# Kernel tuning notes

Hardware: AMD Instinct MI355X
Metric: run time of the kernel (lower is better)

## Reference

```python
import jax, jax.numpy as jnp
import numpy as np

N_NODES = 100000
N_EDGES = 1600000
NODES_PER_GRAPH = 100  # equal-sized graphs -> batch = arange // 100
POOL_K = 30


def setup_inputs() -> dict:
    key = jax.random.key(0)
    ks = jax.random.split(key, 8)
    F_IN, H1, H2, OUT = 128, 128, 128, 64
    x = jax.random.normal(ks[0], (N_NODES, F_IN), dtype=jnp.float32)
    edge_index = jax.random.randint(ks[1], (2, N_EDGES), 0, N_NODES, dtype=jnp.int64)
    batch = (jnp.arange(N_NODES, dtype=jnp.int64) // NODES_PER_GRAPH)
    # Glorot-ish init for weights, zero bias (as PyG GCNConv defaults)
    W1 = jax.random.normal(ks[2], (F_IN, H1), dtype=jnp.float32) / np.sqrt(F_IN)
    b1 = jnp.zeros((H1,), dtype=jnp.float32)
    W2 = jax.random.normal(ks[3], (H1, H2), dtype=jnp.float32) / np.sqrt(H1)
    b2 = jnp.zeros((H2,), dtype=jnp.float32)
    W3 = jax.random.normal(ks[4], (H2, OUT), dtype=jnp.float32) / np.sqrt(H2)
    b3 = jnp.zeros((OUT,), dtype=jnp.float32)
    return {"x": x, "edge_index": edge_index, "batch": batch,
            "W1": W1, "b1": b1, "W2": W2, "b2": b2, "W3": W3, "b3": b3}


def _gcn_conv(x, src, dst, W, b):
    """PyG GCNConv: xW, add self-loops, symmetric D^-1/2 A D^-1/2 scatter-add, +bias."""
    n = x.shape[0]
    loops = jnp.arange(n, dtype=src.dtype)
    row = jnp.concatenate([src, loops])  # message source
    col = jnp.concatenate([dst, loops])  # aggregation target
    xw = x @ W
    deg = jax.ops.segment_sum(jnp.ones(col.shape[0], x.dtype), col, num_segments=n)
    dinv = jnp.where(deg > 0, jax.lax.rsqrt(deg), 0.0)
    norm = dinv[row] * dinv[col]  # [E+N]
    out = jax.ops.segment_sum(xw[row] * norm[:, None], col, num_segments=n)
    return out + b


def _sort_pool(x, k):
    """global_sort_pool: per-graph descending sort by last channel, take top-k, flatten.
    Graphs are equal-sized and contiguous, so reshape to [B, P, C]."""
    n, c = x.shape
    xb = x.reshape(n // NODES_PER_GRAPH, NODES_PER_GRAPH, c)  # [B, P, C]
    order = jnp.argsort(-xb[..., -1], axis=1)[:, :k]          # [B, k]
    topk = jnp.take_along_axis(xb, order[..., None], axis=1)  # [B, k, C]
    return topk.reshape(topk.shape[0], k * c)


def reference(x, edge_index, batch, W1, b1, W2, b2, W3, b3):
    src, dst = edge_index[0], edge_index[1]
    h = jax.nn.relu(_gcn_conv(x, src, dst, W1, b1))
    h = jax.nn.relu(_gcn_conv(h, src, dst, W2, b2))
    h = _gcn_conv(h, src, dst, W3, b3)
    return _sort_pool(h, POOL_K)
```

## Files before the change

### kernel.cpp

```cpp
#include <hip/hip_runtime.h>
#include <math.h>

static inline size_t ws_align(size_t x) { return (x + 255) & ~(size_t)255; }

__global__ void count_kernel(const int* __restrict__ dst, int* __restrict__ counts, int E) {
  int e = blockIdx.x * 256 + threadIdx.x;
  if (e < E) atomicAdd(&counts[dst[e]], 1);
}

__global__ __launch_bounds__(1024) void scan_kernel(const int* __restrict__ counts,
    int* __restrict__ offsets, int* __restrict__ cursor, double* __restrict__ dinv, int n) {
  __shared__ int warpsums[16];
  __shared__ int s_carry;
  int tid = threadIdx.x;
  int lane = tid & 63, wid = tid >> 6;
  if (tid == 0) s_carry = 0;
  __syncthreads();
  for (int base = 0; base < n; base += 1024) {
    int i = base + tid;
    int v = (i < n) ? counts[i] : 0;
    int x = v;
    #pragma unroll
    for (int d = 1; d < 64; d <<= 1) {
      int y = __shfl_up(x, d, 64);
      if (lane >= d) x += y;
    }
    if (lane == 63) warpsums[wid] = x;
    __syncthreads();
    if (wid == 0) {
      int w = (lane < 16) ? warpsums[lane] : 0;
      #pragma unroll
      for (int d = 1; d < 16; d <<= 1) {
        int y = __shfl_up(w, d, 64);
        if (lane >= d) w += y;
      }
      if (lane < 16) warpsums[lane] = w;
    }
    __syncthreads();
    int excl = s_carry + x - v + (wid > 0 ? warpsums[wid - 1] : 0);
    if (i < n) {
      offsets[i] = excl;
      cursor[i] = excl;
      dinv[i] = 1.0 / sqrt((double)(v + 1));
    }
    __syncthreads();
    if (tid == 0) s_carry += warpsums[15];
    __syncthreads();
  }
  if (tid == 0) offsets[n] = s_carry;
}

__global__ void scatter_kernel(const int* __restrict__ src, const int* __restrict__ dst,
    int* __restrict__ cursor, int* __restrict__ srcs, int E) {
  int e = blockIdx.x * 256 + threadIdx.x;
  if (e < E) {
    int p = atomicAdd(&cursor[dst[e]], 1);
    srcs[p] = src[e];
  }
}

template<int H>
__global__ __launch_bounds__(256) void gemm_kernel(const float* __restrict__ X,
    const float* __restrict__ W, float* __restrict__ out, int N) {
  __shared__ float xs[128][68];
  const int tid  = threadIdx.x;
  const int row0 = blockIdx.x * 64;
  #pragma unroll
  for (int p = 0; p < 8; ++p) {
    int idx = p * 256 + tid;
    int r = idx >> 5;
    int c4 = idx & 31;
    int grow = row0 + r;
    float4 v = make_float4(0.f, 0.f, 0.f, 0.f);
    if (grow < N) v = *(const float4*)(X + (size_t)grow * 128 + c4 * 4);
    xs[c4 * 4 + 0][r] = v.x;
    xs[c4 * 4 + 1][r] = v.y;
    xs[c4 * 4 + 2][r] = v.z;
    xs[c4 * 4 + 3][r] = v.w;
  }
  __syncthreads();
  constexpr int CPT = H / 16;
  const int rowg = tid & 15;
  const int colg = tid >> 4;
  double acc[4][CPT];
  #pragma unroll
  for (int j = 0; j < 4; ++j)
    #pragma unroll
    for (int h = 0; h < CPT; ++h) acc[j][h] = 0.0;

  #pragma unroll 4
  for (int k = 0; k < 128; k += 2) {
    float4 av0 = *(const float4*)(&xs[k][rowg * 4]);
    float4 av1 = *(const float4*)(&xs[k + 1][rowg * 4]);
    double a0[4], a1[4];
    a0[0] = (double)av0.x; a0[1] = (double)av0.y; a0[2] = (double)av0.z; a0[3] = (double)av0.w;
    a1[0] = (double)av1.x; a1[1] = (double)av1.y; a1[2] = (double)av1.z; a1[3] = (double)av1.w;
    double b0[CPT], b1[CPT];
    const float* w0 = W + (size_t)k * H + colg * CPT;
    const float* w1 = w0 + H;
    #pragma unroll
    for (int q = 0; q < CPT / 4; ++q) {
      float4 v0 = *(const float4*)(w0 + q * 4);
      float4 v1 = *(const float4*)(w1 + q * 4);
      b0[q*4+0] = (double)v0.x; b0[q*4+1] = (double)v0.y;
      b0[q*4+2] = (double)v0.z; b0[q*4+3] = (double)v0.w;
      b1[q*4+0] = (double)v1.x; b1[q*4+1] = (double)v1.y;
      b1[q*4+2] = (double)v1.z; b1[q*4+3] = (double)v1.w;
    }
    #pragma unroll
    for (int j = 0; j < 4; ++j)
      #pragma unroll
      for (int h = 0; h < CPT; ++h) {
        acc[j][h] = fma(a0[j], b0[h], acc[j][h]);
        acc[j][h] = fma(a1[j], b1[h], acc[j][h]);
      }
  }
  #pragma unroll
  for (int j = 0; j < 4; ++j) {
    int grow = row0 + rowg * 4 + j;
    if (grow < N) {
      float* o = out + (size_t)grow * H + colg * CPT;
      #pragma unroll
      for (int q = 0; q < CPT / 4; ++q) {
        float4 v = make_float4((float)acc[j][q*4+0], (float)acc[j][q*4+1],
                               (float)acc[j][q*4+2], (float)acc[j][q*4+3]);
        *(float4*)(o + q * 4) = v;
      }
    }
  }
}

template<int C, bool RELU>
__global__ __launch_bounds__(256) void gather_kernel(const float* __restrict__ xw,
    const double* __restrict__ dinv, const int* __restrict__ offs,
    const int* __restrict__ srcs, const float* __restrict__ bias,
    float* __restrict__ out, int N) {
  constexpr int LPR = C / 4;
  constexpr int EPI = 64 / LPR;
  const int node = blockIdx.x * 4 + (threadIdx.x >> 6);
  if (node >= N) return;
  const int lane = threadIdx.x & 63;
  const int grp  = lane / LPR;
  const int l    = lane % LPR;
  const int c0   = l * 4;
  const int e0 = offs[node], e1 = offs[node + 1];
  const double di = dinv[node];
  double a0 = 0.0, a1 = 0.0, a2 = 0.0, a3 = 0.0;

  for (int base = e0; base < e1; base += 4 * EPI) {
    int ss[4];
    #pragma unroll
    for (int u = 0; u < 4; ++u) {
      int ee = base + u * EPI + grp;
      ss[u] = srcs[ee < e1 ? ee : e1 - 1];
    }
    float4 vv[4];
    double ww[4];
    #pragma unroll
    for (int u = 0; u < 4; ++u) {
      vv[u] = *(const float4*)(xw + (size_t)ss[u] * C + c0);
      ww[u] = dinv[ss[u]];
    }
    #pragma unroll
    for (int u = 0; u < 4; ++u) {
      int ee = base + u * EPI + grp;
      double w = (ee < e1) ? ww[u] : 0.0;
      a0 = fma(w, (double)vv[u].x, a0);
      a1 = fma(w, (double)vv[u].y, a1);
      a2 = fma(w, (double)vv[u].z, a2);
      a3 = fma(w, (double)vv[u].w, a3);
    }
  }
  #pragma unroll
  for (int m = LPR; m < 64; m <<= 1) {
    a0 += __shfl_xor(a0, m, 64);
    a1 += __shfl_xor(a1, m, 64);
    a2 += __shfl_xor(a2, m, 64);
    a3 += __shfl_xor(a3, m, 64);
  }
  if (grp == 0) {
    const double d2 = di * di;
    float4 sv = *(const float4*)(xw + (size_t)node * C + c0);
    float4 bv = *(const float4*)(bias + c0);
    double o0 = fma(di, a0, fma(d2, (double)sv.x, (double)bv.x));
    double o1 = fma(di, a1, fma(d2, (double)sv.y, (double)bv.y));
    double o2 = fma(di, a2, fma(d2, (double)sv.z, (double)bv.z));
    double o3 = fma(di, a3, fma(d2, (double)sv.w, (double)bv.w));
    if (RELU) {
      o0 = o0 > 0.0 ? o0 : 0.0; o1 = o1 > 0.0 ? o1 : 0.0;
      o2 = o2 > 0.0 ? o2 : 0.0; o3 = o3 > 0.0 ? o3 : 0.0;
    }
    *(float4*)(out + (size_t)node * C + c0) =
        make_float4((float)o0, (float)o1, (float)o2, (float)o3);
  }
}

__global__ __launch_bounds__(128) void sortpool_kernel(const float* __restrict__ h,
    float* __restrict__ out) {
  __shared__ float sv[128];
  __shared__ int si[128];
  int g = blockIdx.x;
  int tid = threadIdx.x;
  const float* hg = h + (size_t)g * 100 * 64;
  if (tid < 100) {
    sv[tid] = hg[tid * 64 + 63];
    si[tid] = tid;
  } else {
    sv[tid] = -3.0e38f;
    si[tid] = 1 << 30;
  }
  __syncthreads();
  for (int k = 2; k <= 128; k <<= 1) {
    for (int j = k >> 1; j > 0; j >>= 1) {
      int i = tid;
      int l = i ^ j;
      if (l > i) {
        float va = sv[i], vb = sv[l];
        int ia = si[i], ib = si[l];
        bool a_before_b = (va > vb) || (va == vb && ia < ib);
        bool up = ((i & k) == 0);
        bool sw = up ? !a_before_b : a_before_b;
        if (sw) { sv[i] = vb; sv[l] = va; si[i] = ib; si[l] = ia; }
      }
      __syncthreads();
    }
  }
  for (int t = tid; t < 30 * 64; t += 128) {
    int kk = t >> 6;
    int c = t & 63;
    out[(size_t)g * (30 * 64) + t] = hg[si[kk] * 64 + c];
  }
}

extern "C" void kernel_launch(void* const* d_in, const int* in_sizes, int n_in,
                              void* d_out, int out_size, void* d_ws, size_t ws_size,
                              hipStream_t stream) {
  const float* x  = (const float*)d_in[0];
  const int*   ei = (const int*)d_in[1];
  const float* W1 = (const float*)d_in[3];
  const float* b1 = (const float*)d_in[4];
  const float* W2 = (const float*)d_in[5];
  const float* b2 = (const float*)d_in[6];
  const float* W3 = (const float*)d_in[7];
  const float* b3 = (const float*)d_in[8];

  const int N = in_sizes[0] / 128;
  const int E = in_sizes[1] / 2;
  const int* src = ei;
  const int* dst = ei + E;
  (void)n_in; (void)out_size; (void)ws_size;

  char* ws = (char*)d_ws;
  size_t off = 0;
  auto alloc = [&](size_t bytes) { char* p = ws + off; off = ws_align(off + bytes); return p; };
  float*  xw      = (float*) alloc((size_t)N * 128 * 4);
  float*  h       = (float*) alloc((size_t)N * 128 * 4);
  double* dinv    = (double*)alloc((size_t)N * 8);
  int*    offsets = (int*)   alloc(((size_t)N + 1) * 4);
  int*    cursor  = (int*)   alloc((size_t)N * 4);
  int*    counts  = (int*)   alloc((size_t)N * 4);
  int*    srcs    = (int*)   alloc((size_t)E * 4);

  hipMemsetAsync(counts, 0, (size_t)N * 4, stream);
  count_kernel<<<(E + 255) / 256, 256, 0, stream>>>(dst, counts, E);
  scan_kernel<<<1, 1024, 0, stream>>>(counts, offsets, cursor, dinv, N);
  scatter_kernel<<<(E + 255) / 256, 256, 0, stream>>>(src, dst, cursor, srcs, E);

  const int gblocks  = (N + 63) / 64;
  const int nblocks4 = (N + 3) / 4;

  gemm_kernel<128><<<gblocks, 256, 0, stream>>>(x, W1, xw, N);
  gather_kernel<128, true ><<<nblocks4, 256, 0, stream>>>(xw, dinv, offsets, srcs, b1, h, N);
  gemm_kernel<128><<<gblocks, 256, 0, stream>>>(h, W2, xw, N);
  gather_kernel<128, true ><<<nblocks4, 256, 0, stream>>>(xw, dinv, offsets, srcs, b2, h, N);
  gemm_kernel<64 ><<<gblocks, 256, 0, stream>>>(h, W3, xw, N);
  gather_kernel<64,  false><<<nblocks4, 256, 0, stream>>>(xw, dinv, offsets, srcs, b3, h, N);
  sortpool_kernel<<<N / 100, 128, 0, stream>>>(h, (float*)d_out);
}
```

Measured before the change: 995.0 us.

## Parallelize CSR scan, precompute edge weights, pre-convert weights to double, unroll gather

```diff
diff --git a/kernel.cpp b/kernel.cpp
--- a/kernel.cpp
+++ b/kernel.cpp
@@ -8,60 +8,95 @@
   if (e < E) atomicAdd(&counts[dst[e]], 1);
 }
 
-__global__ __launch_bounds__(1024) void scan_kernel(const int* __restrict__ counts,
-    int* __restrict__ offsets, int* __restrict__ cursor, double* __restrict__ dinv, int n) {
+__global__ __launch_bounds__(256) void scanA_kernel(const int* __restrict__ counts,
+    int* __restrict__ bsums, int n) {
+  __shared__ int red[4];
+  const int base = blockIdx.x * 1024;
+  const int tid = threadIdx.x;
+  int s = 0;
+  #pragma unroll
+  for (int u = 0; u < 4; ++u) {
+    int i = base + u * 256 + tid;
+    s += (i < n) ? counts[i] : 0;
+  }
+  #pragma unroll
+  for (int m = 1; m < 64; m <<= 1) s += __shfl_xor(s, m, 64);
+  if ((tid & 63) == 0) red[tid >> 6] = s;
+  __syncthreads();
+  if (tid == 0) bsums[blockIdx.x] = red[0] + red[1] + red[2] + red[3];
+}
+
+__global__ __launch_bounds__(128) void scanB_kernel(int* __restrict__ bsums, int nb) {
+  __shared__ int tmp[129];
+  int tid = threadIdx.x;
+  tmp[tid] = (tid < nb) ? bsums[tid] : 0;
+  __syncthreads();
+  if (tid == 0) {
+    int run = 0;
+    for (int i = 0; i < nb; ++i) { int v = tmp[i]; tmp[i] = run; run += v; }
+  }
+  __syncthreads();
+  if (tid < nb) bsums[tid] = tmp[tid];
+}
+
+__global__ __launch_bounds__(1024) void scanC_kernel(const int* __restrict__ counts,
+    const int* __restrict__ bsums, int* __restrict__ offsets, int* __restrict__ cursor,
+    double* __restrict__ dinv, int n) {
   __shared__ int warpsums[16];
-  __shared__ int s_carry;
-  int tid = threadIdx.x;
-  int lane = tid & 63, wid = tid >> 6;
-  if (tid == 0) s_carry = 0;
-  __syncthreads();
-  for (int base = 0; base < n; base += 1024) {
-    int i = base + tid;
-    int v = (i < n) ? counts[i] : 0;
-    int x = v;
-    #pragma unroll
-    for (int d = 1; d < 64; d <<= 1) {
-      int y = __shfl_up(x, d, 64);
-      if (lane >= d) x += y;
-    }
-    if (lane == 63) warpsums[wid] = x;
-    __syncthreads();
-    if (wid == 0) {
-      int w = (lane < 16) ? warpsums[lane] : 0;
-      #pragma unroll
-      for (int d = 1; d < 16; d <<= 1) {
-        int y = __shfl_up(w, d, 64);
-        if (lane >= d) w += y;
-      }
-      if (lane < 16) warpsums[lane] = w;
-    }
-    __syncthreads();
-    int excl = s_carry + x - v + (wid > 0 ? warpsums[wid - 1] : 0);
-    if (i < n) {
-      offsets[i] = excl;
-      cursor[i] = excl;
-      dinv[i] = 1.0 / sqrt((double)(v + 1));
-    }
-    __syncthreads();
-    if (tid == 0) s_carry += warpsums[15];
-    __syncthreads();
-  }
-  if (tid == 0) offsets[n] = s_carry;
+  const int tid = threadIdx.x;
+  const int lane = tid & 63, wid = tid >> 6;
+  const int i = blockIdx.x * 1024 + tid;
+  int v = (i < n) ? counts[i] : 0;
+  int x = v;
+  #pragma unroll
+  for (int d = 1; d < 64; d <<= 1) {
+    int y = __shfl_up(x, d, 64);
+    if (lane >= d) x += y;
+  }
+  if (lane == 63) warpsums[wid] = x;
+  __syncthreads();
+  if (wid == 0) {
+    int w = (lane < 16) ? warpsums[lane] : 0;
+    #pragma unroll
+    for (int d = 1; d < 16; d <<= 1) {
+      int y = __shfl_up(w, d, 64);
+      if (lane >= d) w += y;
+    }
+    if (lane < 16) warpsums[lane] = w;
+  }
+  __syncthreads();
+  int excl = bsums[blockIdx.x] + x - v + (wid > 0 ? warpsums[wid - 1] : 0);
+  if (i < n) {
+    offsets[i] = excl;
+    cursor[i] = excl;
+    dinv[i] = 1.0 / sqrt((double)(v + 1));
+    if (i == n - 1) offsets[n] = excl + v;
+  }
 }
 
 __global__ void scatter_kernel(const int* __restrict__ src, const int* __restrict__ dst,
-    int* __restrict__ cursor, int* __restrict__ srcs, int E) {
+    int* __restrict__ cursor, int* __restrict__ srcs, double* __restrict__ ew,
+    const double* __restrict__ dinv, int E, int use_ew) {
   int e = blockIdx.x * 256 + threadIdx.x;
   if (e < E) {
-    int p = atomicAdd(&cursor[dst[e]], 1);
-    srcs[p] = src[e];
-  }
+    int s = src[e], d = dst[e];
+    int p = atomicAdd(&cursor[d], 1);
+    srcs[p] = s;
+    if (use_ew) ew[p] = dinv[s] * dinv[d];
+  }
+}
+
+__global__ void cvtW_kernel(const float* __restrict__ W1, const float* __restrict__ W2,
+    const float* __restrict__ W3, double* __restrict__ W1d, double* __restrict__ W2d,
+    double* __restrict__ W3d) {
+  int i = blockIdx.x * 256 + threadIdx.x;
+  if (i < 16384) { W1d[i] = (double)W1[i]; W2d[i] = (double)W2[i]; }
+  if (i < 8192)  { W3d[i] = (double)W3[i]; }
 }
 
 template<int H>
 __global__ __launch_bounds__(256) void gemm_kernel(const float* __restrict__ X,
-    const float* __restrict__ W, float* __restrict__ out, int N) {
+    const double* __restrict__ Wd, float* __restrict__ out, int N) {
   __shared__ float xs[128][68];
   const int tid  = threadIdx.x;
   const int row0 = blockIdx.x * 64;
@@ -88,7 +123,7 @@
     #pragma unroll
     for (int h = 0; h < CPT; ++h) acc[j][h] = 0.0;
 
-  #pragma unroll 4
+  #pragma unroll 2
   for (int k = 0; k < 128; k += 2) {
     float4 av0 = *(const float4*)(&xs[k][rowg * 4]);
     float4 av1 = *(const float4*)(&xs[k + 1][rowg * 4]);
@@ -96,16 +131,14 @@
     a0[0] = (double)av0.x; a0[1] = (double)av0.y; a0[2] = (double)av0.z; a0[3] = (double)av0.w;
     a1[0] = (double)av1.x; a1[1] = (double)av1.y; a1[2] = (double)av1.z; a1[3] = (double)av1.w;
     double b0[CPT], b1[CPT];
-    const float* w0 = W + (size_t)k * H + colg * CPT;
-    const float* w1 = w0 + H;
-    #pragma unroll
-    for (int q = 0; q < CPT / 4; ++q) {
-      float4 v0 = *(const float4*)(w0 + q * 4);
-      float4 v1 = *(const float4*)(w1 + q * 4);
-      b0[q*4+0] = (double)v0.x; b0[q*4+1] = (double)v0.y;
-      b0[q*4+2] = (double)v0.z; b0[q*4+3] = (double)v0.w;
-      b1[q*4+0] = (double)v1.x; b1[q*4+1] = (double)v1.y;
-      b1[q*4+2] = (double)v1.z; b1[q*4+3] = (double)v1.w;
+    const double* w0 = Wd + (size_t)k * H + colg * CPT;
+    const double* w1 = w0 + H;
+    #pragma unroll
+    for (int q = 0; q < CPT / 2; ++q) {
+      double2 v0 = *(const double2*)(w0 + q * 2);
+      double2 v1 = *(const double2*)(w1 + q * 2);
+      b0[q*2+0] = v0.x; b0[q*2+1] = v0.y;
+      b1[q*2+0] = v1.x; b1[q*2+1] = v1.y;
     }
     #pragma unroll
     for (int j = 0; j < 4; ++j)
@@ -130,39 +163,41 @@
   }
 }
 
-template<int C, bool RELU>
+template<int C, bool RELU, bool USE_EW>
 __global__ __launch_bounds__(256) void gather_kernel(const float* __restrict__ xw,
     const double* __restrict__ dinv, const int* __restrict__ offs,
-    const int* __restrict__ srcs, const float* __restrict__ bias,
-    float* __restrict__ out, int N) {
+    const int* __restrict__ srcs, const double* __restrict__ ew,
+    const float* __restrict__ bias, float* __restrict__ out, int N) {
   constexpr int LPR = C / 4;
   constexpr int EPI = 64 / LPR;
+  constexpr int U = 8;
   const int node = blockIdx.x * 4 + (threadIdx.x >> 6);
   if (node >= N) return;
   const int lane = threadIdx.x & 63;
   const int grp  = lane / LPR;
-  const int l    = lane % LPR;
-  const int c0   = l * 4;
+  const int c0   = (lane % LPR) * 4;
   const int e0 = offs[node], e1 = offs[node + 1];
   const double di = dinv[node];
   double a0 = 0.0, a1 = 0.0, a2 = 0.0, a3 = 0.0;
 
-  for (int base = e0; base < e1; base += 4 * EPI) {
-    int ss[4];
-    #pragma unroll
-    for (int u = 0; u < 4; ++u) {
+  for (int base = e0; base < e1; base += U * EPI) {
+    int ss[U];
+    double ww[U];
+    float4 vv[U];
+    #pragma unroll
+    for (int u = 0; u < U; ++u) {
       int ee = base + u * EPI + grp;
-      ss[u] = srcs[ee < e1 ? ee : e1 - 1];
-    }
-    float4 vv[4];
-    double ww[4];
-    #pragma unroll
-    for (int u = 0; u < 4; ++u) {
+      int cl = ee < e1 ? ee : e1 - 1;
+      ss[u] = srcs[cl];
+      if (USE_EW) ww[u] = ew[cl];
+    }
+    #pragma unroll
+    for (int u = 0; u < U; ++u) {
       vv[u] = *(const float4*)(xw + (size_t)ss[u] * C + c0);
-      ww[u] = dinv[ss[u]];
-    }
-    #pragma unroll
-    for (int u = 0; u < 4; ++u) {
+      if (!USE_EW) ww[u] = dinv[ss[u]];
+    }
+    #pragma unroll
+    for (int u = 0; u < U; ++u) {
       int ee = base + u * EPI + grp;
       double w = (ee < e1) ? ww[u] : 0.0;
       a0 = fma(w, (double)vv[u].x, a0);
@@ -182,10 +217,18 @@
     const double d2 = di * di;
     float4 sv = *(const float4*)(xw + (size_t)node * C + c0);
     float4 bv = *(const float4*)(bias + c0);
-    double o0 = fma(di, a0, fma(d2, (double)sv.x, (double)bv.x));
-    double o1 = fma(di, a1, fma(d2, (double)sv.y, (double)bv.y));
-    double o2 = fma(di, a2, fma(d2, (double)sv.z, (double)bv.z));
-    double o3 = fma(di, a3, fma(d2, (double)sv.w, (double)bv.w));
+    double o0, o1, o2, o3;
+    if (USE_EW) {
+      o0 = a0 + fma(d2, (double)sv.x, (double)bv.x);
+      o1 = a1 + fma(d2, (double)sv.y, (double)bv.y);
+      o2 = a2 + fma(d2, (double)sv.z, (double)bv.z);
+      o3 = a3 + fma(d2, (double)sv.w, (double)bv.w);
+    } else {
+      o0 = fma(di, a0, fma(d2, (double)sv.x, (double)bv.x));
+      o1 = fma(di, a1, fma(d2, (double)sv.y, (double)bv.y));
+      o2 = fma(di, a2, fma(d2, (double)sv.z, (double)bv.z));
+      o3 = fma(di, a3, fma(d2, (double)sv.w, (double)bv.w));
+    }
     if (RELU) {
       o0 = o0 > 0.0 ? o0 : 0.0; o1 = o1 > 0.0 ? o1 : 0.0;
       o2 = o2 > 0.0 ? o2 : 0.0; o3 = o3 > 0.0 ? o3 : 0.0;
@@ -248,7 +291,9 @@
   const int E = in_sizes[1] / 2;
   const int* src = ei;
   const int* dst = ei + E;
-  (void)n_in; (void)out_size; (void)ws_size;
+  (void)n_in; (void)out_size;
+
+  const int nb = (N + 1023) / 1024;
 
   char* ws = (char*)d_ws;
   size_t off = 0;
@@ -260,20 +305,37 @@
   int*    cursor  = (int*)   alloc((size_t)N * 4);
   int*    counts  = (int*)   alloc((size_t)N * 4);
   int*    srcs    = (int*)   alloc((size_t)E * 4);
+  double* W1d     = (double*)alloc(16384 * 8);
+  double* W2d     = (double*)alloc(16384 * 8);
+  double* W3d     = (double*)alloc(8192 * 8);
+  int*    bsums   = (int*)   alloc((size_t)(nb + 1) * 4);
+  double* ew      = (double*)alloc((size_t)E * 8);
+  const bool use_ew = (off <= ws_size);
 
   hipMemsetAsync(counts, 0, (size_t)N * 4, stream);
   count_kernel<<<(E + 255) / 256, 256, 0, stream>>>(dst, counts, E);
-  scan_kernel<<<1, 1024, 0, stream>>>(counts, offsets, cursor, dinv, N);
-  scatter_kernel<<<(E + 255) / 256, 256, 0, stream>>>(src, dst, cursor, srcs, E);
+  scanA_kernel<<<nb, 256, 0, stream>>>(counts, bsums, N);
+  scanB_kernel<<<1, 128, 0, stream>>>(bsums, nb);
+  scanC_kernel<<<nb, 1024, 0, stream>>>(counts, bsums, offsets, cursor, dinv, N);
+  scatter_kernel<<<(E + 255) / 256, 256, 0, stream>>>(src, dst, cursor, srcs, ew, dinv, E, use_ew ? 1 : 0);
+  cvtW_kernel<<<64, 256, 0, stream>>>(W1, W2, W3, W1d, W2d, W3d);
 
   const int gblocks  = (N + 63) / 64;
   const int nblocks4 = (N + 3) / 4;
 
-  gemm_kernel<128><<<gblocks, 256, 0, stream>>>(x, W1, xw, N);
-  gather_kernel<128, true ><<<nblocks4, 256, 0, stream>>>(xw, dinv, offsets, srcs, b1, h, N);
-  gemm_kernel<128><<<gblocks, 256, 0, stream>>>(h, W2, xw, N);
-  gather_kernel<128, true ><<<nblocks4, 256, 0, stream>>>(xw, dinv, offsets, srcs, b2, h, N);
-  gemm_kernel<64 ><<<gblocks, 256, 0, stream>>>(h, W3, xw, N);
-  gather_kernel<64,  false><<<nblocks4, 256, 0, stream>>>(xw, dinv, offsets, srcs, b3, h, N);
+  gemm_kernel<128><<<gblocks, 256, 0, stream>>>(x, W1d, xw, N);
+  if (use_ew) {
+    gather_kernel<128, true,  true><<<nblocks4, 256, 0, stream>>>(xw, dinv, offsets, srcs, ew, b1, h, N);
+    gemm_kernel<128><<<gblocks, 256, 0, stream>>>(h, W2d, xw, N);
+    gather_kernel<128, true,  true><<<nblocks4, 256, 0, stream>>>(xw, dinv, offsets, srcs, ew, b2, h, N);
+    gemm_kernel<64 ><<<gblocks, 256, 0, stream>>>(h, W3d, xw, N);
+    gather_kernel<64,  false, true><<<nblocks4, 256, 0, stream>>>(xw, dinv, offsets, srcs, ew, b3, h, N);
+  } else {
+    gather_kernel<128, true,  false><<<nblocks4, 256, 0, stream>>>(xw, dinv, offsets, srcs, ew, b1, h, N);
+    gemm_kernel<128><<<gblocks, 256, 0, stream>>>(h, W2d, xw, N);
+    gather_kernel<128, true,  false><<<nblocks4, 256, 0, stream>>>(xw, dinv, offsets, srcs, ew, b2, h, N);
+    gemm_kernel<64 ><<<gblocks, 256, 0, stream>>>(h, W3d, xw, N);
+    gather_kernel<64,  false, false><<<nblocks4, 256, 0, stream>>>(xw, dinv, offsets, srcs, ew, b3, h, N);
+  }
   sortpool_kernel<<<N / 100, 128, 0, stream>>>(h, (float*)d_out);
 }
```

Result: faster. 885.4 us (-11.0%).
